# Performance work log

Hardware: AMD Instinct MI355X
Metric: run time of the kernel (lower is better)

Reference implementation:

```python
import jax, jax.numpy as jnp
import numpy as np

B, N, D, R, W, H, I = 256, 2048, 128, 4, 1, 1024, 1024
CI = I + R * D                       # controller input size (1536)
IF = 2 * D * W + 2 * W + 1 + 4 * R + D * R   # interface size (787)
OPI = H + R * D                      # output_proj input (1536)


def _norm(v):
    # F.normalize(dim=-1): x / max(||x||, eps)
    return v / jnp.maximum(jnp.linalg.norm(v, axis=-1, keepdims=True), 1e-12)


def setup_inputs() -> dict:
    key = jax.random.key(0)
    ks = jax.random.split(key, 16)
    u = lambda k, shape, fan: jax.random.uniform(k, shape, jnp.float32, -1.0 / np.sqrt(fan), 1.0 / np.sqrt(fan))
    return {
        "x": jax.random.normal(ks[0], (B, I), jnp.float32),
        "memory": jax.random.normal(ks[1], (N, D), jnp.float32) * np.sqrt(2.0 / (N + D)),  # xavier-ish
        "usage": jax.random.uniform(ks[2], (N,), jnp.float32),          # usage in [0,1)
        "link": jax.random.normal(ks[3], (N, N), jnp.float32) * 0.01,   # non-trivial link state
        "W_ih": u(ks[4], (4 * H, CI), H),
        "W_hh": u(ks[5], (4 * H, H), H),
        "b_ih": u(ks[6], (4 * H,), H),
        "b_hh": u(ks[7], (4 * H,), H),
        "W_if": u(ks[8], (IF, H), H),
        "b_if": u(ks[9], (IF,), H),
        "W_out": u(ks[10], (H, OPI), OPI),
        "b_out": u(ks[11], (H,), OPI),
    }


def reference(x, memory, usage, link, W_ih, W_hh, b_ih, b_hh, W_if, b_if, W_out, b_out):
    # initial uniform read weights (prev state at first step)
    prev_rw = jnp.full((B, R, N), 1.0 / N, x.dtype)
    read_flat = (prev_rw @ memory).reshape(B, -1)                 # (B, R*D)
    cin = jnp.concatenate([x, read_flat], axis=-1)                # (B, CI)

    # single LSTM step, h0 = c0 = 0, torch gate order i,f,g,o
    g = cin @ W_ih.T + b_ih + b_hh
    gi, gf, gg, go = jnp.split(g, 4, axis=-1)
    c = jax.nn.sigmoid(gi) * jnp.tanh(gg)
    h = jax.nn.sigmoid(go) * jnp.tanh(c)                          # (B, H) controller out

    itf = h @ W_if.T + b_if                                       # (B, IF)
    o = 0
    write_vals = itf[:, o:o + D * W].reshape(B, W, D); o += D * W
    erase = jax.nn.sigmoid(itf[:, o:o + D * W]).reshape(B, W, D); o += D * W
    write_gates = jax.nn.sigmoid(itf[:, o:o + W]); o += W         # (B, W)
    alloc_gate = jax.nn.sigmoid(itf[:, o:o + 1]); o += 1          # (B, 1)
    o += W                                                        # free gates (parsed, unused)
    read_modes = jax.nn.softmax(itf[:, o:o + 3 * R].reshape(B, R, 3), -1); o += 3 * R
    read_str = jax.nn.softplus(itf[:, o:o + R]); o += R           # (B, R)
    read_keys = itf[:, o:o + D * R].reshape(B, R, D)

    # content addressing for the write (strength = 1)
    mem_n = _norm(memory)
    cw = jax.nn.softmax(_norm(write_vals.mean(1)) @ mem_n.T, -1)  # (B, N)

    # allocation weighting: sorted-usage cumprod (per source semantics)
    idx = jnp.argsort(usage)
    su = usage[idx]
    cp = jnp.cumprod(1.0 - su)
    alloc_s = jnp.concatenate([su[:1], su[1:] * cp[:-1]])
    alloc = jnp.zeros_like(usage).at[idx].set(alloc_s)[None, :] * alloc_gate  # (B, N)

    write_w = write_gates[:, :, None] * (0.5 * cw + 0.5 * alloc)[:, None, :]  # (B, W, N)

    # temporal link update: batch-mean of diag-masked outer product, decay 0.9
    lu = jnp.einsum('bwn,bwm->nm', write_w, write_w) / B
    lu = lu * (1.0 - jnp.eye(N, dtype=lu.dtype))
    link_new = link * 0.9 + lu * 0.1

    # memory write (erase then add, batch-mean)
    ev = erase * write_gates[:, :, None]
    av = write_vals * write_gates[:, :, None]
    erase_mat = jnp.einsum('bwn,bwd->nd', write_w, ev) / B
    add_mat = jnp.einsum('bwn,bwd->nd', write_w, av) / B
    mem_new = memory * (1.0 - erase_mat) + add_mat

    # read addressing on updated memory and updated link (all R heads vectorized)
    sim = jnp.einsum('brd,nd->brn', _norm(read_keys), _norm(mem_new))
    content_r = jax.nn.softmax(sim * read_str[:, :, None], -1)    # (B, R, N)
    backward_w = jnp.einsum('brn,nm->brm', prev_rw, link_new)     # mode 1: prev @ L
    forward_w = jnp.einsum('brn,mn->brm', prev_rw, link_new)      # mode 2: prev @ L^T
    new_rw = (read_modes[..., 0:1] * content_r
              + read_modes[..., 1:2] * backward_w
              + read_modes[..., 2:3] * forward_w)                 # (B, R, N)

    read_out = (new_rw @ mem_new).reshape(B, -1)                  # (B, R*D)
    out = jnp.concatenate([h, read_out], axis=-1) @ W_out.T + b_out
    return out
```

## Files before the change

kernel.cpp:

```cpp
#include <hip/hip_runtime.h>
#include <cmath>

#define DEVI __device__ __forceinline__

DEVI float sigm(float x){ return 1.f/(1.f+expf(-x)); }

typedef __attribute__((ext_vector_type(8))) _Float16 half8;
typedef __attribute__((ext_vector_type(4))) _Float16 half4;
typedef __attribute__((ext_vector_type(4))) float float4v;


__global__ void k_zero(float* __restrict__ p, int n){
  int i = blockIdx.x*256 + threadIdx.x;
  if (i < n) p[i] = 0.f;
}

__global__ void k_cast3(const float* __restrict__ a, _Float16* __restrict__ ah, int n1,
                        const float* __restrict__ b, _Float16* __restrict__ bh, int n2,
                        const float* __restrict__ c, _Float16* __restrict__ ch, int n3){
  int i = blockIdx.x*256 + threadIdx.x;
  const float* src; _Float16* dst; int off;
  if (i < n1){ src=a; dst=ah; off=i; }
  else if (i < n1+n2){ src=b; dst=bh; off=i-n1; }
  else if (i < n1+n2+n3){ src=c; dst=ch; off=i-n1-n2; }
  else return;
  const float* p = src + (size_t)off*8;
  half8 h;
  #pragma unroll
  for (int j = 0; j < 8; j++) h[j] = (_Float16)p[j];
  *(half8*)(dst + (size_t)off*8) = h;
}

__global__ __launch_bounds__(256) void k_prep_mem(const float* __restrict__ mem,
    float* __restrict__ cm, _Float16* __restrict__ mem_h){
  __shared__ float s2[4][128];
  int tid = threadIdx.x, wv = tid >> 6, lane = tid & 63;
  int n0 = blockIdx.x*64;
  float c0 = 0.f, c1 = 0.f;
  for (int r = wv; r < 64; r += 4){
    const float* a = mem + (size_t)(n0+r)*128;
    float x0 = a[lane], x1 = a[lane+64];
    float ss = x0*x0 + x1*x1;
    #pragma unroll
    for (int o = 1; o < 64; o <<= 1) ss += __shfl_xor(ss, o);
    float invn = 1.f / fmaxf(sqrtf(ss), 1e-12f);
    mem_h[(size_t)(n0+r)*128 + lane]      = (_Float16)(x0*invn);
    mem_h[(size_t)(n0+r)*128 + 64 + lane] = (_Float16)(x1*invn);
    c0 += x0; c1 += x1;
  }
  s2[wv][lane] = c0; s2[wv][64+lane] = c1;
  __syncthreads();
  if (tid < 128) atomicAdd(&cm[tid], s2[0][tid]+s2[1][tid]+s2[2][tid]+s2[3][tid]);
}

__global__ void k_cin(const float* __restrict__ x, const float* __restrict__ cm, _Float16* __restrict__ cin){
  int idx = blockIdx.x*256 + threadIdx.x;
  int b = idx / 1536, k = idx - b*1536;
  float v = (k < 1024) ? x[b*1024 + k] : cm[(k-1024) & 127] * (1.f/2048.f);
  cin[idx] = (_Float16)v;
}

#define QA 264
#define QB 520
__global__ __launch_bounds__(256) void gemm_f16(
    const _Float16* __restrict__ A, const _Float16* __restrict__ Bm, float* __restrict__ C,
    int M, int N, int K,
    const float* __restrict__ bias1, const float* __restrict__ bias2)
{
  __shared__ _Float16 Ah[2][8*QA];
  __shared__ _Float16 Bh[2][8*QB];
  const int tid = threadIdx.x;
  const int m0 = blockIdx.y*32, n0 = blockIdx.x*64;
  const int T = K >> 6;
  const int arow = tid >> 3, aq = tid & 7;
  const _Float16* Aptr = A + (size_t)(m0 + arow)*K + aq*8;
  const int brow = tid >> 3, bq = tid & 7;
  int nB0 = n0 + brow;      if (nB0 >= N) nB0 = N - 1;
  int nB1 = n0 + brow + 32; if (nB1 >= N) nB1 = N - 1;
  const _Float16* Bptr0 = Bm + (size_t)nB0*K + bq*8;
  const _Float16* Bptr1 = Bm + (size_t)nB1*K + bq*8;
  const int wA  = aq*QA + arow*8;
  const int wB0 = bq*QB + brow*8;
  const int wB1 = bq*QB + (brow+32)*8;
  const int wv_ = tid >> 6, lane = tid & 63;
  const int fq = lane >> 4, fr = lane & 15;
  const int m16 = (wv_ & 1)*16, nb = (wv_ >> 1)*32;

  half8 ra, rb0, rb1;
  ra  = *(const half8*)(Aptr);
  rb0 = *(const half8*)(Bptr0);
  rb1 = *(const half8*)(Bptr1);
  *(half8*)&Ah[0][wA]  = ra;
  *(half8*)&Bh[0][wB0] = rb0;
  *(half8*)&Bh[0][wB1] = rb1;
  __syncthreads();

  float4v acc0 = {0.f,0.f,0.f,0.f}, acc1 = {0.f,0.f,0.f,0.f};
  for (int t = 0; t < T; t++){
    const int cur = t & 1, nxt = cur ^ 1;
    if (t+1 < T){
      ra  = *(const half8*)(Aptr  + (t+1)*64);
      rb0 = *(const half8*)(Bptr0 + (t+1)*64);
      rb1 = *(const half8*)(Bptr1 + (t+1)*64);
    }
    #pragma unroll
    for (int s = 0; s < 2; s++){
      int q = s*4 + fq;
      half8 a  = *(half8*)&Ah[cur][q*QA + (m16+fr)*8];
      half8 b0 = *(half8*)&Bh[cur][q*QB + (nb+fr)*8];
      half8 b1 = *(half8*)&Bh[cur][q*QB + (nb+16+fr)*8];
      acc0 = __builtin_amdgcn_mfma_f32_16x16x32_f16(a, b0, acc0, 0, 0, 0);
      acc1 = __builtin_amdgcn_mfma_f32_16x16x32_f16(a, b1, acc1, 0, 0, 0);
    }
    if (t+1 < T){
      *(half8*)&Ah[nxt][wA]  = ra;
      *(half8*)&Bh[nxt][wB0] = rb0;
      *(half8*)&Bh[nxt][wB1] = rb1;
    }
    __syncthreads();
  }

  const int colA = n0 + nb + fr, colB = colA + 16;
  #pragma unroll
  for (int i = 0; i < 4; i++){
    int m = m0 + m16 + fq*4 + i;
    if (colA < N){
      float v = acc0[i];
      if (bias1) v += bias1[colA];
      if (bias2) v += bias2[colA];
      C[(size_t)m*N + colA] = v;
    }
    if (colB < N){
      float v = acc1[i];
      if (bias1) v += bias1[colB];
      if (bias2) v += bias2[colB];
      C[(size_t)m*N + colB] = v;
    }
  }
}

__global__ void k_lstm(const float* __restrict__ g, _Float16* __restrict__ h){
  int idx = blockIdx.x*256 + threadIdx.x;
  int b = idx >> 10, j = idx & 1023;
  const float* gr = g + (size_t)b*4096;
  float c = sigm(gr[j]) * tanhf(gr[2048 + j]);
  h[idx] = (_Float16)(sigm(gr[3072 + j]) * tanhf(c));
}

DEVI float blockReduce128(float v, float* lds2){
  #pragma unroll
  for (int o = 32; o > 0; o >>= 1) v += __shfl_xor(v, o);
  int w = threadIdx.x >> 6;
  __syncthreads();
  if ((threadIdx.x & 63) == 0) lds2[w] = v;
  __syncthreads();
  return lds2[0] + lds2[1];
}

__global__ __launch_bounds__(128) void k_parse(const float* __restrict__ itf,
    _Float16* __restrict__ wv_h, float* __restrict__ ev, float* __restrict__ av,
    float* __restrict__ wg_, float* __restrict__ ag_,
    float* __restrict__ rm0, float* __restrict__ rm1, float* __restrict__ rm2,
    _Float16* __restrict__ rks_h)
{
  __shared__ float red[2];
  int b = blockIdx.x, t = threadIdx.x;
  const float* it = itf + (size_t)b*787;
  float wg = sigm(it[256]);
  float ag = sigm(it[257]);
  if (t == 0){ wg_[b] = wg; ag_[b] = ag; }
  float w = it[t];
  av[b*128 + t] = w * wg;
  ev[b*128 + t] = sigm(it[128 + t]) * wg;
  float ss = blockReduce128(w*w, red);
  float invwv = 1.f / fmaxf(sqrtf(ss), 1e-12f);
  wv_h[b*128 + t] = (_Float16)(w * invwv);
  if (t < 4){
    int rr = t;
    float m0v = it[259 + rr*3 + 0], m1v = it[259 + rr*3 + 1], m2v = it[259 + rr*3 + 2];
    float mx = fmaxf(m0v, fmaxf(m1v, m2v));
    float e0 = expf(m0v - mx), e1 = expf(m1v - mx), e2 = expf(m2v - mx);
    float inv = 1.f / (e0 + e1 + e2);
    rm0[b*4 + rr] = e0*inv; rm1[b*4 + rr] = e1*inv; rm2[b*4 + rr] = e2*inv;
  }
  #pragma unroll
  for (int rr = 0; rr < 4; rr++){
    float kv = it[275 + rr*128 + t];
    float ks = blockReduce128(kv*kv, red);
    float sx = it[271 + rr];
    float str = fmaxf(sx, 0.f) + log1pf(expf(-fabsf(sx)));
    float invk = 1.f / fmaxf(sqrtf(ks), 1e-12f);
    rks_h[((size_t)b*4 + rr)*128 + t] = (_Float16)(kv * invk * str);
  }
}

__global__ __launch_bounds__(256) void k_alloc(const float* __restrict__ usage, float* __restrict__ out){
  __shared__ float red[4];
  int n = blockIdx.x, t = threadIdx.x;
  float un = usage[n];
  float prod = 1.f;
  #pragma unroll
  for (int i = 0; i < 8; i++){
    int m = t + i*256;
    float um = usage[m];
    bool before = (um < un) || (um == un && m < n);
    prod *= before ? (1.f - um) : 1.f;
  }
  #pragma unroll
  for (int o = 32; o > 0; o >>= 1) prod *= __shfl_xor(prod, o);
  if ((t & 63) == 0) red[t >> 6] = prod;
  __syncthreads();
  if (t == 0) out[n] = un * (red[0]*red[1]) * (red[2]*red[3]);
}

__global__ __launch_bounds__(256) void k_softmax_ww(float* __restrict__ P,
    const float* __restrict__ alloc, const float* __restrict__ wg, const float* __restrict__ ag){
  __shared__ float red[4];
  float* p = P + (size_t)blockIdx.x*2048;
  int t = threadIdx.x;
  float r[8];
  float mx = -3.4e38f;
  #pragma unroll
  for (int i = 0; i < 8; i++){ r[i] = p[t + i*256]; mx = fmaxf(mx, r[i]); }
  #pragma unroll
  for (int o = 32; o > 0; o >>= 1) mx = fmaxf(mx, __shfl_xor(mx, o));
  if ((t & 63) == 0) red[t >> 6] = mx;
  __syncthreads();
  mx = fmaxf(fmaxf(red[0], red[1]), fmaxf(red[2], red[3]));
  float s = 0.f;
  #pragma unroll
  for (int i = 0; i < 8; i++){ r[i] = expf(r[i] - mx); s += r[i]; }
  #pragma unroll
  for (int o = 32; o > 0; o >>= 1) s += __shfl_xor(s, o);
  __syncthreads();
  if ((t & 63) == 0) red[t >> 6] = s;
  __syncthreads();
  s = red[0] + red[1] + red[2] + red[3];
  float inv = 1.f / s;
  float wgb = wg[blockIdx.x], agb = ag[blockIdx.x];
  #pragma unroll
  for (int i = 0; i < 8; i++){
    int col = t + i*256;
    p[col] = wgb*(0.5f*r[i]*inv + 0.5f*alloc[col]*agb);
  }
}

__global__ void k_rowsum(const float* __restrict__ A, float* __restrict__ out, int rows, int cols){
  int w = (blockIdx.x*blockDim.x + threadIdx.x) >> 6;
  int lane = threadIdx.x & 63;
  if (w >= rows) return;
  const float* a = A + (size_t)w*cols;
  float s = 0.f;
  for (int c = lane; c < cols; c += 64) s += a[c];
  #pragma unroll
  for (int o = 32; o > 0; o >>= 1) s += __shfl_down(s, o);
  if (lane == 0) out[w] = s;
}

__global__ void k_colsum2048(const float* __restrict__ A, float* __restrict__ out){
  int c = blockIdx.x*256 + threadIdx.x;
  int r0 = blockIdx.y*128;
  float s = 0.f;
  for (int rr = 0; rr < 128; rr++) s += A[(size_t)(r0+rr)*2048 + c];
  atomicAdd(&out[c], s);
}

__global__ __launch_bounds__(1024) void k_bwfw(const float* __restrict__ ww, const float* __restrict__ tb,
                       const float* __restrict__ rowsum, const float* __restrict__ colsum,
                       float* __restrict__ bw, float* __restrict__ fw){
  __shared__ float sq[4][256], sd[4][256];
  int t = threadIdx.x & 255, z = threadIdx.x >> 8;
  int m = blockIdx.x*256 + t;
  float q = 0.f, dd = 0.f;
  for (int b = z*64; b < z*64 + 64; b++){
    float w = ww[(size_t)b*2048 + m];
    q  = fmaf(tb[b], w, q);
    dd = fmaf(w, w, dd);
  }
  sq[z][t] = q; sd[z][t] = dd;
  __syncthreads();
  if (z == 0){
    q  = sq[0][t] + sq[1][t] + sq[2][t] + sq[3][t];
    dd = sd[0][t] + sd[1][t] + sd[2][t] + sd[3][t];
    float lus = (q - dd) * (1.f/256.f);
    bw[m] = (0.9f*colsum[m] + 0.1f*lus) * (1.f/2048.f);
    fw[m] = (0.9f*rowsum[m] + 0.1f*lus) * (1.f/2048.f);
  }
}

__global__ __launch_bounds__(256) void k_memupdate_fused(const float* __restrict__ ww,
    const float* __restrict__ ev, const float* __restrict__ av,
    const float* __restrict__ mem, const float* __restrict__ bw, const float* __restrict__ fw,
    _Float16* __restrict__ memn_h, _Float16* __restrict__ memnraw_h,
    float* __restrict__ bwm, float* __restrict__ fwm)
{
  __shared__ float Ws[16][34];
  __shared__ float Es[16][132], Vs[16][132];
  __shared__ float lb[128], lf[128];
  const int n0 = blockIdx.x*32;
  const int tid = threadIdx.x, tx = tid & 31, ty = tid >> 5;
  if (tid < 128){ lb[tid] = 0.f; lf[tid] = 0.f; }
  const int wk = tid >> 4, wn = (tid & 15)*2;
  const int ek = tid >> 4, ec = (tid & 15)*8;
  float ae[4][4] = {}, aa[4][4] = {};
  for (int k0 = 0; k0 < 256; k0 += 16){
    float2 vw  = *(const float2*)(ww + (size_t)(k0+wk)*2048 + n0 + wn);
    float4 ve0 = *(const float4*)(ev + (size_t)(k0+ek)*128 + ec);
    float4 ve1 = *(const float4*)(ev + (size_t)(k0+ek)*128 + ec + 4);
    float4 va0 = *(const float4*)(av + (size_t)(k0+ek)*128 + ec);
    float4 va1 = *(const float4*)(av + (size_t)(k0+ek)*128 + ec + 4);
    __syncthreads();
    Ws[wk][wn] = vw.x; Ws[wk][wn+1] = vw.y;
    *(float4*)&Es[ek][ec] = ve0; *(float4*)&Es[ek][ec+4] = ve1;
    *(float4*)&Vs[ek][ec] = va0; *(float4*)&Vs[ek][ec+4] = va1;
    __syncthreads();
    #pragma unroll
    for (int k = 0; k < 16; k++){
      float a[4], e[4], v[4];
      #pragma unroll
      for (int i = 0; i < 4; i++) a[i] = Ws[k][ty*4+i];
      #pragma unroll
      for (int j = 0; j < 4; j++){ e[j] = Es[k][tx*4+j]; v[j] = Vs[k][tx*4+j]; }
      #pragma unroll
      for (int i = 0; i < 4; i++)
        #pragma unroll
        for (int j = 0; j < 4; j++){
          ae[i][j] = fmaf(a[i], e[j], ae[i][j]);
          aa[i][j] = fmaf(a[i], v[j], aa[i][j]);
        }
    }
  }
  float ab[4] = {0,0,0,0}, af[4] = {0,0,0,0};
  #pragma unroll
  for (int i = 0; i < 4; i++){
    int n = n0 + ty*4 + i;
    float bwn = bw[n], fwn = fw[n];
    float v[4]; float ss = 0.f;
    #pragma unroll
    for (int j = 0; j < 4; j++){
      int d = tx*4 + j;
      float em = ae[i][j]*(1.f/256.f), am = aa[i][j]*(1.f/256.f);
      float mv = mem[(size_t)n*128 + d]*(1.f - em) + am;
      v[j] = mv; ss += mv*mv;
      ab[j] = fmaf(bwn, mv, ab[j]);
      af[j] = fmaf(fwn, mv, af[j]);
    }
    #pragma unroll
    for (int o = 1; o < 32; o <<= 1) ss += __shfl_xor(ss, o);
    float invn = 1.f / fmaxf(sqrtf(ss), 1e-12f);
    half4 hn, hr;
    #pragma unroll
    for (int j = 0; j < 4; j++){ hn[j] = (_Float16)(v[j]*invn); hr[j] = (_Float16)v[j]; }
    *(half4*)(memn_h    + (size_t)n*128 + tx*4) = hn;
    *(half4*)(memnraw_h + (size_t)n*128 + tx*4) = hr;
  }
  __syncthreads();
  #pragma unroll
  for (int j = 0; j < 4; j++){
    atomicAdd(&lb[tx*4+j], ab[j]);
    atomicAdd(&lf[tx*4+j], af[j]);
  }
  __syncthreads();
  if (tid < 128){
    atomicAdd(&bwm[tid], lb[tid]);
    atomicAdd(&fwm[tid], lf[tid]);
  }
}

__global__ __launch_bounds__(256) void k_transpose(const _Float16* __restrict__ src,
                                                   _Float16* __restrict__ dst){
  __shared__ _Float16 T[32][136];
  int tid = threadIdx.x;
  int k0 = blockIdx.x*32;
  int rk = tid >> 3, cc = (tid & 7)*16;
  *(half8*)&T[rk][cc]   = *(const half8*)(src + (size_t)(k0+rk)*128 + cc);
  *(half8*)&T[rk][cc+8] = *(const half8*)(src + (size_t)(k0+rk)*128 + cc + 8);
  __syncthreads();
  int d = tid >> 1, kk = (tid & 1)*16;
  half8 o0, o1;
  #pragma unroll
  for (int j = 0; j < 8; j++){ o0[j] = T[kk+j][d]; o1[j] = T[kk+8+j][d]; }
  *(half8*)(dst + (size_t)d*2048 + k0 + kk)     = o0;
  *(half8*)(dst + (size_t)d*2048 + k0 + kk + 8) = o1;
}

__global__ __launch_bounds__(256) void k_flash(
    const _Float16* __restrict__ Q, const _Float16* __restrict__ Kh,
    const _Float16* __restrict__ Vt,
    float* __restrict__ pacc, float* __restrict__ pm, float* __restrict__ pl)
{
  __shared__ _Float16 Pl[4][16][32];
  __shared__ float cmb[4][2080];
  __shared__ float scl[4][16];
  const int tid = threadIdx.x;
  const int qt = blockIdx.x >> 2, kc = blockIdx.x & 3;
  const int wv = tid >> 6, lane = tid & 63;
  const int fq = lane >> 4, fr = lane & 15;
  const int kw0 = kc*512 + wv*128;

  half8 aq[4];
  #pragma unroll
  for (int c = 0; c < 4; c++)
    aq[c] = *(const half8*)(Q + (size_t)(qt*16 + fr)*128 + c*32 + fq*8);

  float m[4] = {-3.0e38f,-3.0e38f,-3.0e38f,-3.0e38f};
  float l[4] = {0.f,0.f,0.f,0.f};
  float4v acc[8] = {};
  for (int s = 0; s < 4; s++){
    const int kb = kw0 + s*32;
    float4v S0 = {0,0,0,0}, S1 = {0,0,0,0};
    #pragma unroll
    for (int c = 0; c < 4; c++){
      half8 b0 = *(const half8*)(Kh + (size_t)(kb + fr)*128      + c*32 + fq*8);
      half8 b1 = *(const half8*)(Kh + (size_t)(kb + 16 + fr)*128 + c*32 + fq*8);
      S0 = __builtin_amdgcn_mfma_f32_16x16x32_f16(aq[c], b0, S0, 0, 0, 0);
      S1 = __builtin_amdgcn_mfma_f32_16x16x32_f16(aq[c], b1, S1, 0, 0, 0);
    }
    float mt[4], ps[4];
    #pragma unroll
    for (int i = 0; i < 4; i++) mt[i] = fmaxf(S0[i], S1[i]);
    #pragma unroll
    for (int o = 1; o < 16; o <<= 1){
      #pragma unroll
      for (int i = 0; i < 4; i++) mt[i] = fmaxf(mt[i], __shfl_xor(mt[i], o));
    }
    #pragma unroll
    for (int i = 0; i < 4; i++){
      float mn = fmaxf(m[i], mt[i]);
      float al = expf(m[i] - mn);
      float p0 = expf(S0[i] - mn), p1 = expf(S1[i] - mn);
      S0[i] = p0; S1[i] = p1;
      ps[i] = p0 + p1;
      l[i] *= al;
      m[i] = mn;
      #pragma unroll
      for (int c = 0; c < 8; c++) acc[c][i] *= al;
    }
    #pragma unroll
    for (int o = 1; o < 16; o <<= 1){
      #pragma unroll
      for (int i = 0; i < 4; i++) ps[i] += __shfl_xor(ps[i], o);
    }
    #pragma unroll
    for (int i = 0; i < 4; i++) l[i] += ps[i];
    #pragma unroll
    for (int i = 0; i < 4; i++){
      Pl[wv][fq*4+i][fr]      = (_Float16)S0[i];
      Pl[wv][fq*4+i][16 + fr] = (_Float16)S1[i];
    }
    half8 pf = *(half8*)&Pl[wv][fr][fq*8];
    #pragma unroll
    for (int c = 0; c < 8; c++){
      half8 bv = *(const half8*)(Vt + (size_t)(c*16 + fr)*2048 + kb + fq*8);
      acc[c] = __builtin_amdgcn_mfma_f32_16x16x32_f16(pf, bv, acc[c], 0, 0, 0);
    }
  }
  if (fr == 0){
    #pragma unroll
    for (int i = 0; i < 4; i++){
      cmb[wv][fq*4+i]      = m[i];
      cmb[wv][16 + fq*4+i] = l[i];
    }
  }
  #pragma unroll
  for (int c = 0; c < 8; c++)
    #pragma unroll
    for (int i = 0; i < 4; i++)
      cmb[wv][32 + (fq*4+i)*128 + c*16 + fr] = acc[c][i];
  __syncthreads();
  if (tid < 16){
    float mm = fmaxf(fmaxf(cmb[0][tid], cmb[1][tid]), fmaxf(cmb[2][tid], cmb[3][tid]));
    float ll = 0.f;
    #pragma unroll
    for (int w = 0; w < 4; w++){
      float e = expf(cmb[w][tid] - mm);
      scl[w][tid] = e;
      ll += e * cmb[w][16 + tid];
    }
    pm[blockIdx.x*16 + tid] = mm;
    pl[blockIdx.x*16 + tid] = ll;
  }
  __syncthreads();
  for (int e = tid; e < 2048; e += 256){
    int q = e >> 7;
    float a = scl[0][q]*cmb[0][32+e] + scl[1][q]*cmb[1][32+e]
            + scl[2][q]*cmb[2][32+e] + scl[3][q]*cmb[3][32+e];
    pacc[(size_t)blockIdx.x*2048 + e] = a;
  }
}

__global__ void k_flashcomb(const float* __restrict__ pacc, const float* __restrict__ pm,
                            const float* __restrict__ pl,
                            const float* __restrict__ rm0, const float* __restrict__ rm1,
                            const float* __restrict__ rm2, const float* __restrict__ bwm,
                            const float* __restrict__ fwm, float* __restrict__ ro){
  int idx = blockIdx.x*256 + threadIdx.x;
  int row = idx >> 7, d = idx & 127;
  int qt = row >> 4, q = row & 15;
  float mm = -3.0e38f;
  #pragma unroll
  for (int kc = 0; kc < 4; kc++) mm = fmaxf(mm, pm[(qt*4+kc)*16 + q]);
  float num = 0.f, den = 0.f;
  #pragma unroll
  for (int kc = 0; kc < 4; kc++){
    float e = expf(pm[(qt*4+kc)*16 + q] - mm);
    den += e * pl[(qt*4+kc)*16 + q];
    num += e * pacc[(size_t)(qt*4+kc)*2048 + q*128 + d];
  }
  float pv = num / den;
  ro[idx] = rm0[row]*pv + rm1[row]*bwm[d] + rm2[row]*fwm[d];
}

__global__ void k_hro(const _Float16* __restrict__ h, const float* __restrict__ ro, _Float16* __restrict__ hro){
  int idx = blockIdx.x*256 + threadIdx.x;
  int b = idx / 1536, k = idx - b*1536;
  hro[idx] = (k < 1024) ? h[b*1024 + k] : (_Float16)ro[b*512 + k - 1024];
}


extern "C" void kernel_launch(void* const* d_in, const int* in_sizes, int n_in,
                              void* d_out, int out_size, void* d_ws, size_t ws_size,
                              hipStream_t stream)
{
  const float* x     = (const float*)d_in[0];
  const float* mem   = (const float*)d_in[1];
  const float* usage = (const float*)d_in[2];
  const float* link  = (const float*)d_in[3];
  const float* W_ih  = (const float*)d_in[4];
  const float* b_ih  = (const float*)d_in[6];
  const float* b_hh  = (const float*)d_in[7];
  const float* W_if  = (const float*)d_in[8];
  const float* b_if  = (const float*)d_in[9];
  const float* W_out = (const float*)d_in[10];
  const float* b_out = (const float*)d_in[11];
  float* out = (float*)d_out;
  float* ws  = (float*)d_ws;

  float* cm     = ws + 0;
  float* csl    = ws + 128;
  float* bwm    = ws + 2176;
  float* fwm    = ws + 2304;
  float* tb     = ws + 2432;
  float* bw     = ws + 2688;
  float* fw     = ws + 4736;
  float* wg     = ws + 6784;
  float* ag     = ws + 7040;
  float* rm0    = ws + 7296;
  float* rm1    = ws + 8320;
  float* rm2    = ws + 9344;
  float* alloc  = ws + 10368;
  float* rsl    = ws + 12416;
  float* ev     = ws + 14464;
  float* av     = ws + 47232;
  float* g      = ws + 80000;
  float* itf    = ws + 1128576;
  float* ww     = ws + 1330048;
  float* ro     = ws + 1854336;
  float* pacc = g;
  float* pm   = g + 524288;
  float* pl   = g + 528384;
  _Float16* Wih_h     = (_Float16*)(ws + 1985408);
  _Float16* Wif_h     = (_Float16*)(ws + 5131136);
  _Float16* Wout_h    = (_Float16*)(ws + 5534080);
  _Float16* cin_h     = (_Float16*)(ws + 6320512);
  _Float16* h_h       = (_Float16*)(ws + 6517120);
  _Float16* hro_h     = (_Float16*)(ws + 6648192);
  _Float16* wv_h      = (_Float16*)(ws + 6844800);
  _Float16* mem_h     = (_Float16*)(ws + 6861184);
  _Float16* memn_h    = (_Float16*)(ws + 6992256);
  _Float16* memnraw_h = (_Float16*)(ws + 7123328);
  _Float16* memnT_h   = (_Float16*)(ws + 7254400);
  _Float16* rks_h     = (_Float16*)(ws + 7385472);

  k_zero <<<10, 256, 0, stream>>>(ws, 2432);
  k_cast3<<<4234, 256, 0, stream>>>(W_ih, Wih_h, 786432, W_if, Wif_h, 100736, W_out, Wout_h, 196608);

  k_prep_mem<<<32, 256, 0, stream>>>(mem, cm, mem_h);
  k_cin     <<<1536, 256, 0, stream>>>(x, cm, cin_h);

  gemm_f16<<<dim3(64,8), 256, 0, stream>>>(cin_h, Wih_h, g, 256, 4096, 1536, b_ih, b_hh);
  k_lstm  <<<1024, 256, 0, stream>>>(g, h_h);

  gemm_f16<<<dim3(13,8), 256, 0, stream>>>(h_h, Wif_h, itf, 256, 787, 1024, b_if, nullptr);
  k_parse <<<256, 128, 0, stream>>>(itf, wv_h, ev, av, wg, ag, rm0, rm1, rm2, rks_h);

  k_alloc<<<2048, 256, 0, stream>>>(usage, alloc);
  gemm_f16<<<dim3(32,8), 256, 0, stream>>>(wv_h, mem_h, ww, 256, 2048, 128, nullptr, nullptr);
  k_softmax_ww<<<256, 256, 0, stream>>>(ww, alloc, wg, ag);

  k_rowsum<<<512, 256, 0, stream>>>(link, rsl, 2048, 2048);
  k_colsum2048<<<dim3(8,16), 256, 0, stream>>>(link, csl);
  k_rowsum<<<64, 256, 0, stream>>>(ww, tb, 256, 2048);
  k_bwfw  <<<8, 1024, 0, stream>>>(ww, tb, rsl, csl, bw, fw);

  k_memupdate_fused<<<64, 256, 0, stream>>>(ww, ev, av, mem, bw, fw, memn_h, memnraw_h, bwm, fwm);
  k_transpose<<<64, 256, 0, stream>>>(memnraw_h, memnT_h);

  k_flash    <<<256, 256, 0, stream>>>(rks_h, memn_h, memnT_h, pacc, pm, pl);
  k_flashcomb<<<512, 256, 0, stream>>>(pacc, pm, pl, rm0, rm1, rm2, bwm, fwm, ro);

  k_hro   <<<1536, 256, 0, stream>>>(h_h, ro, hro_h);
  gemm_f16<<<dim3(16,8), 256, 0, stream>>>(hro_h, Wout_h, out, 256, 1024, 1536, b_out, nullptr);

  (void)in_sizes; (void)n_in; (void)out_size; (void)ws_size;
}
```

Before: 280.3 us.

## Fuse weight casts into GEMM loads and merge small kernels into fewer launches

Removes the separate fp32-to-fp16 weight cast kernel: the GEMMs now read fp32 weights and convert on load, and build the A operand on the fly (cin from x and the memory column mean, h from LSTM gates). Prep, allocation and link row/column sums are merged into one multi-role kernel. The transpose is folded into the memory update, and the flash combine into the hro builder. The row-sum of ww is replaced by the algebraic identity wg*(0.5+0.5*ag*sum(alloc)). This cuts launches and intermediate traffic, but the GEMMs now move twice the weight bytes and recompute the LSTM transcendentals redundantly for every N-tile.

```diff
diff --git a/kernel.cpp b/kernel.cpp
--- a/kernel.cpp
+++ b/kernel.cpp
@@ -15,57 +15,127 @@
   if (i < n) p[i] = 0.f;
 }
 
-__global__ void k_cast3(const float* __restrict__ a, _Float16* __restrict__ ah, int n1,
-                        const float* __restrict__ b, _Float16* __restrict__ bh, int n2,
-                        const float* __restrict__ c, _Float16* __restrict__ ch, int n3){
-  int i = blockIdx.x*256 + threadIdx.x;
-  const float* src; _Float16* dst; int off;
-  if (i < n1){ src=a; dst=ah; off=i; }
-  else if (i < n1+n2){ src=b; dst=bh; off=i-n1; }
-  else if (i < n1+n2+n3){ src=c; dst=ch; off=i-n1-n2; }
-  else return;
-  const float* p = src + (size_t)off*8;
+DEVI half8 f8_to_h8(const float* p){
+  float4v a = *(const float4v*)p;
+  float4v b = *(const float4v*)(p+4);
   half8 h;
   #pragma unroll
-  for (int j = 0; j < 8; j++) h[j] = (_Float16)p[j];
-  *(half8*)(dst + (size_t)off*8) = h;
-}
-
-__global__ __launch_bounds__(256) void k_prep_mem(const float* __restrict__ mem,
-    float* __restrict__ cm, _Float16* __restrict__ mem_h){
-  __shared__ float s2[4][128];
-  int tid = threadIdx.x, wv = tid >> 6, lane = tid & 63;
-  int n0 = blockIdx.x*64;
-  float c0 = 0.f, c1 = 0.f;
-  for (int r = wv; r < 64; r += 4){
-    const float* a = mem + (size_t)(n0+r)*128;
-    float x0 = a[lane], x1 = a[lane+64];
-    float ss = x0*x0 + x1*x1;
-    #pragma unroll
-    for (int o = 1; o < 64; o <<= 1) ss += __shfl_xor(ss, o);
-    float invn = 1.f / fmaxf(sqrtf(ss), 1e-12f);
-    mem_h[(size_t)(n0+r)*128 + lane]      = (_Float16)(x0*invn);
-    mem_h[(size_t)(n0+r)*128 + 64 + lane] = (_Float16)(x1*invn);
-    c0 += x0; c1 += x1;
-  }
-  s2[wv][lane] = c0; s2[wv][64+lane] = c1;
-  __syncthreads();
-  if (tid < 128) atomicAdd(&cm[tid], s2[0][tid]+s2[1][tid]+s2[2][tid]+s2[3][tid]);
-}
-
-__global__ void k_cin(const float* __restrict__ x, const float* __restrict__ cm, _Float16* __restrict__ cin){
-  int idx = blockIdx.x*256 + threadIdx.x;
-  int b = idx / 1536, k = idx - b*1536;
-  float v = (k < 1024) ? x[b*1024 + k] : cm[(k-1024) & 127] * (1.f/2048.f);
-  cin[idx] = (_Float16)v;
+  for (int j = 0; j < 4; j++){ h[j] = (_Float16)a[j]; h[4+j] = (_Float16)b[j]; }
+  return h;
+}
+
+__global__ __launch_bounds__(256) void k_stage1(
+    const float* __restrict__ mem, float* __restrict__ cm, _Float16* __restrict__ mem_h,
+    const float* __restrict__ usage, float* __restrict__ alloc, float* __restrict__ Sa,
+    const float* __restrict__ link, float* __restrict__ rsl, float* __restrict__ csl)
+{
+  __shared__ float smem[4][132];
+  const int blk = blockIdx.x, t = threadIdx.x;
+  const int wv = t >> 6, lane = t & 63;
+
+  if (blk < 32){
+    int n0 = blk*64;
+    float c0 = 0.f, c1 = 0.f;
+    for (int r = wv; r < 64; r += 4){
+      const float* a = mem + (size_t)(n0+r)*128;
+      float x0 = a[lane], x1 = a[lane+64];
+      float ss = x0*x0 + x1*x1;
+      #pragma unroll
+      for (int o = 1; o < 64; o <<= 1) ss += __shfl_xor(ss, o);
+      float invn = 1.f / fmaxf(sqrtf(ss), 1e-12f);
+      mem_h[(size_t)(n0+r)*128 + lane]      = (_Float16)(x0*invn);
+      mem_h[(size_t)(n0+r)*128 + 64 + lane] = (_Float16)(x1*invn);
+      c0 += x0; c1 += x1;
+    }
+    smem[wv][lane] = c0; smem[wv][64+lane] = c1;
+    __syncthreads();
+    if (t < 128) atomicAdd(&cm[t], smem[0][t]+smem[1][t]+smem[2][t]+smem[3][t]);
+  } else if (blk < 2080){
+    int n = blk - 32;
+    float un = usage[n];
+    float prod = 1.f;
+    #pragma unroll
+    for (int i = 0; i < 8; i++){
+      int m = t + i*256;
+      float um = usage[m];
+      bool before = (um < un) || (um == un && m < n);
+      prod *= before ? (1.f - um) : 1.f;
+    }
+    #pragma unroll
+    for (int o = 32; o > 0; o >>= 1) prod *= __shfl_xor(prod, o);
+    if (lane == 0) smem[0][wv] = prod;
+    __syncthreads();
+    if (t == 0){
+      float v = un * (smem[0][0]*smem[0][1]) * (smem[0][2]*smem[0][3]);
+      alloc[n] = v;
+      atomicAdd(Sa, v);
+    }
+  } else {
+    int r0 = (blk - 2080)*32;
+    int c0 = t*8;
+    float colacc[8];
+    #pragma unroll
+    for (int j = 0; j < 8; j++) colacc[j] = 0.f;
+    for (int r = 0; r < 32; r++){
+      const float* lp = link + (size_t)(r0+r)*2048 + c0;
+      float4v v0 = *(const float4v*)lp;
+      float4v v1 = *(const float4v*)(lp+4);
+      float s = 0.f;
+      #pragma unroll
+      for (int j = 0; j < 4; j++){
+        colacc[j]   += v0[j]; colacc[4+j] += v1[j];
+        s += v0[j] + v1[j];
+      }
+      #pragma unroll
+      for (int o = 32; o > 0; o >>= 1) s += __shfl_xor(s, o);
+      if (lane == 0) smem[wv][r] = s;
+    }
+    __syncthreads();
+    if (t < 32) rsl[r0+t] = smem[0][t]+smem[1][t]+smem[2][t]+smem[3][t];
+    #pragma unroll
+    for (int j = 0; j < 8; j++) atomicAdd(&csl[c0+j], colacc[j]);
+  }
 }
 
 #define QA 264
 #define QB 520
-__global__ __launch_bounds__(256) void gemm_f16(
-    const _Float16* __restrict__ A, const _Float16* __restrict__ Bm, float* __restrict__ C,
+
+template<int AM>
+DEVI half8 loadA(const void* __restrict__ Av, int row, int k, int K, const float* __restrict__ cm){
+  if constexpr (AM == 0){
+    const _Float16* A = (const _Float16*)Av;
+    return *(const half8*)(A + (size_t)row*K + k);
+  } else if constexpr (AM == 1){
+    if (k < 1024) return f8_to_h8((const float*)Av + (size_t)row*1024 + k);
+    const float* p = cm + ((k - 1024) & 127);
+    half8 h;
+    #pragma unroll
+    for (int j = 0; j < 8; j++) h[j] = (_Float16)(p[j] * (1.f/2048.f));
+    return h;
+  } else {
+    const float* gp = (const float*)Av + (size_t)row*4096 + k;
+    half8 h;
+    #pragma unroll
+    for (int j = 0; j < 8; j++){
+      float c = sigm(gp[j]) * tanhf(gp[2048+j]);
+      h[j] = (_Float16)(sigm(gp[3072+j]) * tanhf(c));
+    }
+    return h;
+  }
+}
+
+template<typename TB>
+DEVI half8 ldB8(const TB* __restrict__ p){
+  if constexpr (sizeof(TB) == 2) return *(const half8*)p;
+  else return f8_to_h8((const float*)p);
+}
+
+template<int AM, typename TB>
+__global__ __launch_bounds__(256) void gemm_t(
+    const void* __restrict__ Av, const TB* __restrict__ Bm, float* __restrict__ C,
     int M, int N, int K,
-    const float* __restrict__ bias1, const float* __restrict__ bias2)
+    const float* __restrict__ bias1, const float* __restrict__ bias2,
+    const float* __restrict__ cm)
 {
   __shared__ _Float16 Ah[2][8*QA];
   __shared__ _Float16 Bh[2][8*QB];
@@ -73,23 +143,23 @@
   const int m0 = blockIdx.y*32, n0 = blockIdx.x*64;
   const int T = K >> 6;
   const int arow = tid >> 3, aq = tid & 7;
-  const _Float16* Aptr = A + (size_t)(m0 + arow)*K + aq*8;
   const int brow = tid >> 3, bq = tid & 7;
   int nB0 = n0 + brow;      if (nB0 >= N) nB0 = N - 1;
   int nB1 = n0 + brow + 32; if (nB1 >= N) nB1 = N - 1;
-  const _Float16* Bptr0 = Bm + (size_t)nB0*K + bq*8;
-  const _Float16* Bptr1 = Bm + (size_t)nB1*K + bq*8;
+  const TB* Bp0 = Bm + (size_t)nB0*K + bq*8;
+  const TB* Bp1 = Bm + (size_t)nB1*K + bq*8;
   const int wA  = aq*QA + arow*8;
   const int wB0 = bq*QB + brow*8;
   const int wB1 = bq*QB + (brow+32)*8;
   const int wv_ = tid >> 6, lane = tid & 63;
   const int fq = lane >> 4, fr = lane & 15;
   const int m16 = (wv_ & 1)*16, nb = (wv_ >> 1)*32;
+  const int arw = m0 + arow;
 
   half8 ra, rb0, rb1;
-  ra  = *(const half8*)(Aptr);
-  rb0 = *(const half8*)(Bptr0);
-  rb1 = *(const half8*)(Bptr1);
+  ra  = loadA<AM>(Av, arw, aq*8, K, cm);
+  rb0 = ldB8<TB>(Bp0);
+  rb1 = ldB8<TB>(Bp1);
   *(half8*)&Ah[0][wA]  = ra;
   *(half8*)&Bh[0][wB0] = rb0;
   *(half8*)&Bh[0][wB1] = rb1;
@@ -99,9 +169,9 @@
   for (int t = 0; t < T; t++){
     const int cur = t & 1, nxt = cur ^ 1;
     if (t+1 < T){
-      ra  = *(const half8*)(Aptr  + (t+1)*64);
-      rb0 = *(const half8*)(Bptr0 + (t+1)*64);
-      rb1 = *(const half8*)(Bptr1 + (t+1)*64);
+      ra  = loadA<AM>(Av, arw, aq*8 + (t+1)*64, K, cm);
+      rb0 = ldB8<TB>(Bp0 + (t+1)*64);
+      rb1 = ldB8<TB>(Bp1 + (t+1)*64);
     }
     #pragma unroll
     for (int s = 0; s < 2; s++){
@@ -137,14 +207,6 @@
       C[(size_t)m*N + colB] = v;
     }
   }
-}
-
-__global__ void k_lstm(const float* __restrict__ g, _Float16* __restrict__ h){
-  int idx = blockIdx.x*256 + threadIdx.x;
-  int b = idx >> 10, j = idx & 1023;
-  const float* gr = g + (size_t)b*4096;
-  float c = sigm(gr[j]) * tanhf(gr[2048 + j]);
-  h[idx] = (_Float16)(sigm(gr[3072 + j]) * tanhf(c));
 }
 
 DEVI float blockReduce128(float v, float* lds2){
@@ -194,25 +256,6 @@
   }
 }
 
-__global__ __launch_bounds__(256) void k_alloc(const float* __restrict__ usage, float* __restrict__ out){
-  __shared__ float red[4];
-  int n = blockIdx.x, t = threadIdx.x;
-  float un = usage[n];
-  float prod = 1.f;
-  #pragma unroll
-  for (int i = 0; i < 8; i++){
-    int m = t + i*256;
-    float um = usage[m];
-    bool before = (um < un) || (um == un && m < n);
-    prod *= before ? (1.f - um) : 1.f;
-  }
-  #pragma unroll
-  for (int o = 32; o > 0; o >>= 1) prod *= __shfl_xor(prod, o);
-  if ((t & 63) == 0) red[t >> 6] = prod;
-  __syncthreads();
-  if (t == 0) out[n] = un * (red[0]*red[1]) * (red[2]*red[3]);
-}
-
 __global__ __launch_bounds__(256) void k_softmax_ww(float* __restrict__ P,
     const float* __restrict__ alloc, const float* __restrict__ wg, const float* __restrict__ ag){
   __shared__ float red[4];
@@ -245,36 +288,24 @@
   }
 }
 
-__global__ void k_rowsum(const float* __restrict__ A, float* __restrict__ out, int rows, int cols){
-  int w = (blockIdx.x*blockDim.x + threadIdx.x) >> 6;
-  int lane = threadIdx.x & 63;
-  if (w >= rows) return;
-  const float* a = A + (size_t)w*cols;
-  float s = 0.f;
-  for (int c = lane; c < cols; c += 64) s += a[c];
-  #pragma unroll
-  for (int o = 32; o > 0; o >>= 1) s += __shfl_down(s, o);
-  if (lane == 0) out[w] = s;
-}
-
-__global__ void k_colsum2048(const float* __restrict__ A, float* __restrict__ out){
-  int c = blockIdx.x*256 + threadIdx.x;
-  int r0 = blockIdx.y*128;
-  float s = 0.f;
-  for (int rr = 0; rr < 128; rr++) s += A[(size_t)(r0+rr)*2048 + c];
-  atomicAdd(&out[c], s);
-}
-
-__global__ __launch_bounds__(1024) void k_bwfw(const float* __restrict__ ww, const float* __restrict__ tb,
+__global__ __launch_bounds__(1024) void k_bwfw(const float* __restrict__ ww,
+                       const float* __restrict__ wg, const float* __restrict__ ag,
+                       const float* __restrict__ Sa,
                        const float* __restrict__ rowsum, const float* __restrict__ colsum,
                        float* __restrict__ bw, float* __restrict__ fw){
   __shared__ float sq[4][256], sd[4][256];
+  __shared__ float tbs[256];
   int t = threadIdx.x & 255, z = threadIdx.x >> 8;
   int m = blockIdx.x*256 + t;
+  if (threadIdx.x < 256){
+    float sa = Sa[0];
+    tbs[threadIdx.x] = wg[threadIdx.x]*(0.5f + 0.5f*ag[threadIdx.x]*sa);
+  }
+  __syncthreads();
   float q = 0.f, dd = 0.f;
   for (int b = z*64; b < z*64 + 64; b++){
     float w = ww[(size_t)b*2048 + m];
-    q  = fmaf(tb[b], w, q);
+    q  = fmaf(tbs[b], w, q);
     dd = fmaf(w, w, dd);
   }
   sq[z][t] = q; sd[z][t] = dd;
@@ -291,12 +322,13 @@
 __global__ __launch_bounds__(256) void k_memupdate_fused(const float* __restrict__ ww,
     const float* __restrict__ ev, const float* __restrict__ av,
     const float* __restrict__ mem, const float* __restrict__ bw, const float* __restrict__ fw,
-    _Float16* __restrict__ memn_h, _Float16* __restrict__ memnraw_h,
+    _Float16* __restrict__ memn_h, _Float16* __restrict__ memnT_h,
     float* __restrict__ bwm, float* __restrict__ fwm)
 {
   __shared__ float Ws[16][34];
   __shared__ float Es[16][132], Vs[16][132];
   __shared__ float lb[128], lf[128];
+  __shared__ _Float16 Traw[32][132];
   const int n0 = blockIdx.x*32;
   const int tid = threadIdx.x, tx = tid & 31, ty = tid >> 5;
   if (tid < 128){ lb[tid] = 0.f; lf[tid] = 0.f; }
@@ -351,10 +383,18 @@
     half4 hn, hr;
     #pragma unroll
     for (int j = 0; j < 4; j++){ hn[j] = (_Float16)(v[j]*invn); hr[j] = (_Float16)v[j]; }
-    *(half4*)(memn_h    + (size_t)n*128 + tx*4) = hn;
-    *(half4*)(memnraw_h + (size_t)n*128 + tx*4) = hr;
-  }
-  __syncthreads();
+    *(half4*)(memn_h + (size_t)n*128 + tx*4) = hn;
+    *(half4*)&Traw[ty*4+i][tx*4] = hr;
+  }
+  __syncthreads();
+  {
+    int d = tid >> 1, seg = (tid & 1)*16;
+    half8 o0, o1;
+    #pragma unroll
+    for (int j = 0; j < 8; j++){ o0[j] = Traw[seg+j][d]; o1[j] = Traw[seg+8+j][d]; }
+    *(half8*)(memnT_h + (size_t)d*2048 + n0 + seg)     = o0;
+    *(half8*)(memnT_h + (size_t)d*2048 + n0 + seg + 8) = o1;
+  }
   #pragma unroll
   for (int j = 0; j < 4; j++){
     atomicAdd(&lb[tx*4+j], ab[j]);
@@ -365,23 +405,6 @@
     atomicAdd(&bwm[tid], lb[tid]);
     atomicAdd(&fwm[tid], lf[tid]);
   }
-}
-
-__global__ __launch_bounds__(256) void k_transpose(const _Float16* __restrict__ src,
-                                                   _Float16* __restrict__ dst){
-  __shared__ _Float16 T[32][136];
-  int tid = threadIdx.x;
-  int k0 = blockIdx.x*32;
-  int rk = tid >> 3, cc = (tid & 7)*16;
-  *(half8*)&T[rk][cc]   = *(const half8*)(src + (size_t)(k0+rk)*128 + cc);
-  *(half8*)&T[rk][cc+8] = *(const half8*)(src + (size_t)(k0+rk)*128 + cc + 8);
-  __syncthreads();
-  int d = tid >> 1, kk = (tid & 1)*16;
-  half8 o0, o1;
-  #pragma unroll
-  for (int j = 0; j < 8; j++){ o0[j] = T[kk+j][d]; o1[j] = T[kk+8+j][d]; }
-  *(half8*)(dst + (size_t)d*2048 + k0 + kk)     = o0;
-  *(half8*)(dst + (size_t)d*2048 + k0 + kk + 8) = o1;
 }
 
 __global__ __launch_bounds__(256) void k_flash(
@@ -489,32 +512,33 @@
   }
 }
 
-__global__ void k_flashcomb(const float* __restrict__ pacc, const float* __restrict__ pm,
-                            const float* __restrict__ pl,
-                            const float* __restrict__ rm0, const float* __restrict__ rm1,
-                            const float* __restrict__ rm2, const float* __restrict__ bwm,
-                            const float* __restrict__ fwm, float* __restrict__ ro){
-  int idx = blockIdx.x*256 + threadIdx.x;
-  int row = idx >> 7, d = idx & 127;
-  int qt = row >> 4, q = row & 15;
-  float mm = -3.0e38f;
-  #pragma unroll
-  for (int kc = 0; kc < 4; kc++) mm = fmaxf(mm, pm[(qt*4+kc)*16 + q]);
-  float num = 0.f, den = 0.f;
-  #pragma unroll
-  for (int kc = 0; kc < 4; kc++){
-    float e = expf(pm[(qt*4+kc)*16 + q] - mm);
-    den += e * pl[(qt*4+kc)*16 + q];
-    num += e * pacc[(size_t)(qt*4+kc)*2048 + q*128 + d];
-  }
-  float pv = num / den;
-  ro[idx] = rm0[row]*pv + rm1[row]*bwm[d] + rm2[row]*fwm[d];
-}
-
-__global__ void k_hro(const _Float16* __restrict__ h, const float* __restrict__ ro, _Float16* __restrict__ hro){
+__global__ void k_hro_comb(const float* __restrict__ g, const float* __restrict__ pacc,
+                           const float* __restrict__ pm, const float* __restrict__ pl,
+                           const float* __restrict__ rm0, const float* __restrict__ rm1,
+                           const float* __restrict__ rm2, const float* __restrict__ bwm,
+                           const float* __restrict__ fwm, _Float16* __restrict__ hro){
   int idx = blockIdx.x*256 + threadIdx.x;
   int b = idx / 1536, k = idx - b*1536;
-  hro[idx] = (k < 1024) ? h[b*1024 + k] : (_Float16)ro[b*512 + k - 1024];
+  if (k < 1024){
+    const float* gr = g + (size_t)b*4096;
+    float c = sigm(gr[k]) * tanhf(gr[2048 + k]);
+    hro[idx] = (_Float16)(sigm(gr[3072 + k]) * tanhf(c));
+  } else {
+    int r = k - 1024, rh = r >> 7, d = r & 127;
+    int row = b*4 + rh, qt = row >> 4, q = row & 15;
+    float mm = -3.0e38f;
+    #pragma unroll
+    for (int kc = 0; kc < 4; kc++) mm = fmaxf(mm, pm[(qt*4+kc)*16 + q]);
+    float num = 0.f, den = 0.f;
+    #pragma unroll
+    for (int kc = 0; kc < 4; kc++){
+      float e = expf(pm[(qt*4+kc)*16 + q] - mm);
+      den += e * pl[(qt*4+kc)*16 + q];
+      num += e * pacc[(size_t)(qt*4+kc)*2048 + q*128 + d];
+    }
+    float pv = num / den;
+    hro[idx] = (_Float16)(rm0[row]*pv + rm1[row]*bwm[d] + rm2[row]*fwm[d]);
+  }
 }
 
 
@@ -540,7 +564,7 @@
   float* csl    = ws + 128;
   float* bwm    = ws + 2176;
   float* fwm    = ws + 2304;
-  float* tb     = ws + 2432;
+  float* Sa     = ws + 2432;
   float* bw     = ws + 2688;
   float* fw     = ws + 4736;
   float* wg     = ws + 6784;
@@ -555,52 +579,36 @@
   float* g      = ws + 80000;
   float* itf    = ws + 1128576;
   float* ww     = ws + 1330048;
-  float* ro     = ws + 1854336;
-  float* pacc = g;
-  float* pm   = g + 524288;
-  float* pl   = g + 528384;
-  _Float16* Wih_h     = (_Float16*)(ws + 1985408);
-  _Float16* Wif_h     = (_Float16*)(ws + 5131136);
-  _Float16* Wout_h    = (_Float16*)(ws + 5534080);
-  _Float16* cin_h     = (_Float16*)(ws + 6320512);
-  _Float16* h_h       = (_Float16*)(ws + 6517120);
-  _Float16* hro_h     = (_Float16*)(ws + 6648192);
-  _Float16* wv_h      = (_Float16*)(ws + 6844800);
-  _Float16* mem_h     = (_Float16*)(ws + 6861184);
-  _Float16* memn_h    = (_Float16*)(ws + 6992256);
-  _Float16* memnraw_h = (_Float16*)(ws + 7123328);
-  _Float16* memnT_h   = (_Float16*)(ws + 7254400);
-  _Float16* rks_h     = (_Float16*)(ws + 7385472);
-
-  k_zero <<<10, 256, 0, stream>>>(ws, 2432);
-  k_cast3<<<4234, 256, 0, stream>>>(W_ih, Wih_h, 786432, W_if, Wif_h, 100736, W_out, Wout_h, 196608);
-
-  k_prep_mem<<<32, 256, 0, stream>>>(mem, cm, mem_h);
-  k_cin     <<<1536, 256, 0, stream>>>(x, cm, cin_h);
-
-  gemm_f16<<<dim3(64,8), 256, 0, stream>>>(cin_h, Wih_h, g, 256, 4096, 1536, b_ih, b_hh);
-  k_lstm  <<<1024, 256, 0, stream>>>(g, h_h);
-
-  gemm_f16<<<dim3(13,8), 256, 0, stream>>>(h_h, Wif_h, itf, 256, 787, 1024, b_if, nullptr);
-  k_parse <<<256, 128, 0, stream>>>(itf, wv_h, ev, av, wg, ag, rm0, rm1, rm2, rks_h);
-
-  k_alloc<<<2048, 256, 0, stream>>>(usage, alloc);
-  gemm_f16<<<dim3(32,8), 256, 0, stream>>>(wv_h, mem_h, ww, 256, 2048, 128, nullptr, nullptr);
+  float* pacc   = ws + 1854336;
+  float* pm     = ws + 2378624;
+  float* pl     = ws + 2382720;
+  _Float16* wv_h    = (_Float16*)(ws + 2386816);
+  _Float16* mem_h   = (_Float16*)(ws + 2403200);
+  _Float16* memn_h  = (_Float16*)(ws + 2534272);
+  _Float16* memnT_h = (_Float16*)(ws + 2665344);
+  _Float16* rks_h   = (_Float16*)(ws + 2796416);
+  _Float16* hro_h   = (_Float16*)(ws + 2861952);
+
+  k_zero<<<10, 256, 0, stream>>>(ws, 2433);
+
+  k_stage1<<<2144, 256, 0, stream>>>(mem, cm, mem_h, usage, alloc, Sa, link, rsl, csl);
+
+  gemm_t<1,float><<<dim3(64,8), 256, 0, stream>>>(x, W_ih, g, 256, 4096, 1536, b_ih, b_hh, cm);
+
+  gemm_t<2,float><<<dim3(13,8), 256, 0, stream>>>(g, W_if, itf, 256, 787, 1024, b_if, nullptr, nullptr);
+  k_parse<<<256, 128, 0, stream>>>(itf, wv_h, ev, av, wg, ag, rm0, rm1, rm2, rks_h);
+
+  gemm_t<0,_Float16><<<dim3(32,8), 256, 0, stream>>>(wv_h, mem_h, ww, 256, 2048, 128, nullptr, nullptr, nullptr);
   k_softmax_ww<<<256, 256, 0, stream>>>(ww, alloc, wg, ag);
 
-  k_rowsum<<<512, 256, 0, stream>>>(link, rsl, 2048, 2048);
-  k_colsum2048<<<dim3(8,16), 256, 0, stream>>>(link, csl);
-  k_rowsum<<<64, 256, 0, stream>>>(ww, tb, 256, 2048);
-  k_bwfw  <<<8, 1024, 0, stream>>>(ww, tb, rsl, csl, bw, fw);
-
-  k_memupdate_fused<<<64, 256, 0, stream>>>(ww, ev, av, mem, bw, fw, memn_h, memnraw_h, bwm, fwm);
-  k_transpose<<<64, 256, 0, stream>>>(memnraw_h, memnT_h);
-
-  k_flash    <<<256, 256, 0, stream>>>(rks_h, memn_h, memnT_h, pacc, pm, pl);
-  k_flashcomb<<<512, 256, 0, stream>>>(pacc, pm, pl, rm0, rm1, rm2, bwm, fwm, ro);
-
-  k_hro   <<<1536, 256, 0, stream>>>(h_h, ro, hro_h);
-  gemm_f16<<<dim3(16,8), 256, 0, stream>>>(hro_h, Wout_h, out, 256, 1024, 1536, b_out, nullptr);
+  k_bwfw<<<8, 1024, 0, stream>>>(ww, wg, ag, Sa, rsl, csl, bw, fw);
+
+  k_memupdate_fused<<<64, 256, 0, stream>>>(ww, ev, av, mem, bw, fw, memn_h, memnT_h, bwm, fwm);
+
+  k_flash<<<256, 256, 0, stream>>>(rks_h, memn_h, memnT_h, pacc, pm, pl);
+
+  k_hro_comb<<<1536, 256, 0, stream>>>(g, pacc, pm, pl, rm0, rm1, rm2, bwm, fwm, hro_h);
+  gemm_t<0,float><<<dim3(16,8), 256, 0, stream>>>(hro_h, W_out, out, 256, 1024, 1536, b_out, nullptr, nullptr);
 
   (void)in_sizes; (void)n_in; (void)out_size; (void)ws_size;
 }
```

After: 333.9 us. +19.1%, slower.
